# Optimization experiments

Hardware: AMD Instinct MI355X
Metric: run time of the kernel (lower is better)

## Reference

```python
import jax, jax.numpy as jnp
import numpy as np

RATIO = 0.2
OLD_CL = 11

def setup_inputs() -> dict:
    key = jax.random.key(0)
    inputs = jax.random.normal(key, (8, 19, 512, 1024), dtype=jnp.float32)
    return {"inputs": inputs}

def reference(inputs):
    N, C, H, W = inputs.shape
    probs = jax.nn.softmax(inputs, axis=1)              # (N,C,H,W)
    argpred = jnp.argmax(probs, axis=1)                 # (N,H,W) int
    # Per-image class histogram via one segment_sum: segment id = n*C + class
    flat = argpred.reshape(N, H * W)
    ids = (flat + (jnp.arange(N, dtype=flat.dtype)[:, None] * C)).reshape(-1)
    hist = jax.ops.segment_sum(jnp.ones((N * H * W,), jnp.float32), ids,
                               num_segments=N * C).reshape(N, C)
    hist = jnp.where(hist == 0, 1.0, hist)              # hist[hist==0]=1
    weight = jnp.power(hist.sum(axis=1, keepdims=True) / hist, RATIO)  # (N,C)
    if OLD_CL > 0:
        weight = weight.at[:, :OLD_CL].set(1.0)
    weight = jax.lax.stop_gradient(weight)[:, :, None, None]  # (N,C,1,1), detached
    loss = -(probs * probs) * weight
    return loss.mean()
```

## Files before the change

kernel.cpp:

```cpp
#include <hip/hip_runtime.h>

#define NIMG 8
#define NC 19
#define HW (512*1024)
#define BPI 128
#define TPB 256
#define ITERS 8
#define CPB (ITERS*TPB)
#define OLD_CL 11
#define NWAVE (TPB/64)

typedef float    f32x2 __attribute__((ext_vector_type(2)));
typedef unsigned u32x2 __attribute__((ext_vector_type(2)));

__global__ __launch_bounds__(TPB, 4) void iw_main(const float* __restrict__ in,
                                                  float* __restrict__ sPart,
                                                  unsigned* __restrict__ hPart) {
    const int b   = blockIdx.x;
    const int n   = b >> 7;
    const int bl  = b & (BPI - 1);
    const int tid = threadIdx.x;
    const float* img = in + (size_t)n * NC * HW;

    float    acc[NC];
    unsigned hc[5];
#pragma unroll
    for (int c = 0; c < NC; ++c) acc[c] = 0.f;
#pragma unroll
    for (int r = 0; r < 5; ++r) hc[r] = 0u;

    const float L2E = 1.4426950408889634f;

    for (int it = 0; it < ITERS; ++it) {
        const int    chunk = bl * CPB + it * TPB + tid;
        const size_t p     = (size_t)chunk * 2;

        float x0[NC], x1[NC];
#pragma unroll
        for (int c = 0; c < NC; ++c) {
            const f32x2 t = *reinterpret_cast<const f32x2*>(img + (size_t)c * HW + p);
            x0[c] = t[0]; x1[c] = t[1];
        }

#define PIXEL(X)                                                              \
        {                                                                     \
            float m = X[0];                                                   \
            _Pragma("unroll")                                                 \
            for (int c = 1; c < NC; ++c) m = fmaxf(m, X[c]);                  \
            int mi = NC - 1;                                                  \
            _Pragma("unroll")                                                 \
            for (int c = NC - 2; c >= 0; --c) mi = (X[c] == m) ? c : mi;      \
            {                                                                 \
                const unsigned inc = 1u << ((mi & 3) * 8);                    \
                const int r = mi >> 2;                                        \
                hc[0] += (r == 0) ? inc : 0u;                                 \
                hc[1] += (r == 1) ? inc : 0u;                                 \
                hc[2] += (r == 2) ? inc : 0u;                                 \
                hc[3] += (r == 3) ? inc : 0u;                                 \
                hc[4] += (r == 4) ? inc : 0u;                                 \
            }                                                                 \
            const float ml = m * L2E;                                         \
            float e[NC]; float d = 0.f;                                       \
            _Pragma("unroll")                                                 \
            for (int c = 0; c < NC; ++c) {                                    \
                e[c] = exp2f(fmaf(X[c], L2E, -ml));                           \
                d += e[c];                                                    \
            }                                                                 \
            const float inv  = __builtin_amdgcn_rcpf(d);                      \
            const float inv2 = inv * inv;                                     \
            _Pragma("unroll")                                                 \
            for (int c = 0; c < NC; ++c)                                      \
                acc[c] = fmaf(e[c] * e[c], inv2, acc[c]);                     \
        }

        PIXEL(x0); PIXEL(x1);
#undef PIXEL
    }

    unsigned hu[NC];
#pragma unroll
    for (int c = 0; c < NC; ++c) hu[c] = (hc[c >> 2] >> ((c & 3) * 8)) & 0xFFu;

#pragma unroll
    for (int c = 0; c < NC; ++c) {
#pragma unroll
        for (int off = 32; off >= 1; off >>= 1) {
            acc[c] += __shfl_xor(acc[c], off, 64);
            hu[c]  += (unsigned)__shfl_xor((int)hu[c], off, 64);
        }
    }

    __shared__ float    ls[NWAVE][NC];
    __shared__ unsigned lh[NWAVE][NC];
    const int wave = tid >> 6;
    const int lane = tid & 63;
    if (lane == 0) {
#pragma unroll
        for (int c = 0; c < NC; ++c) { ls[wave][c] = acc[c]; lh[wave][c] = hu[c]; }
    }
    __syncthreads();
    if (tid < NC) {
        float s = 0.f; unsigned h = 0u;
#pragma unroll
        for (int w = 0; w < NWAVE; ++w) { s += ls[w][tid]; h += lh[w][tid]; }
        sPart[(size_t)tid * (NIMG * BPI) + n * BPI + bl] = s;
        hPart[(size_t)tid * (NIMG * BPI) + n * BPI + bl] = h;
    }
}

__global__ __launch_bounds__(1024) void iw_final(const float* __restrict__ sPart,
                                                 const unsigned* __restrict__ hPart,
                                                 float* __restrict__ out) {
    __shared__ float    sRed[NIMG * NC];
    __shared__ unsigned hRed[NIMG * NC];
    __shared__ double contrib[NIMG * NC];
    __shared__ double histL[NIMG * NC];
    __shared__ double hsum[NIMG];

    const int t    = threadIdx.x;
    const int wv   = t >> 6;
    const int lane = t & 63;

#pragma unroll
    for (int i = 0; i < 10; ++i) {
        const int pair = wv + 16 * i;
        if (pair < NIMG * NC) {
            const size_t base = (size_t)pair * BPI + lane * 2;
            const f32x2 sv = *reinterpret_cast<const f32x2*>(sPart + base);
            const u32x2 hv = *reinterpret_cast<const u32x2*>(hPart + base);
            float    s = sv[0] + sv[1];
            unsigned h = hv[0] + hv[1];
#pragma unroll
            for (int off = 32; off >= 1; off >>= 1) {
                s += __shfl_xor(s, off, 64);
                h += (unsigned)__shfl_xor((int)h, off, 64);
            }
            if (lane == 0) { sRed[pair] = s; hRed[pair] = h; }
        }
    }
    __syncthreads();

    if (t < NIMG * NC) {
        const int c = t / NIMG, n = t % NIMG;
        const int idx = n * NC + c;
        const unsigned h = hRed[t];
        histL[idx]   = (h == 0u) ? 1.0 : (double)h;
        contrib[idx] = (double)sRed[t];
    }
    __syncthreads();
    if (t < NIMG) {
        double hs = 0.0;
        for (int c = 0; c < NC; ++c) hs += histL[t * NC + c];
        hsum[t] = hs;
    }
    __syncthreads();
    if (t < NIMG * NC) {
        const int n = t / NC, c = t % NC;
        const double w = (c < OLD_CL) ? 1.0 : pow(hsum[n] / histL[t], 0.2);
        contrib[t] = w * contrib[t];
    }
    __syncthreads();
    if (t == 0) {
        double tot = 0.0;
        for (int i = 0; i < NIMG * NC; ++i) tot += contrib[i];
        out[0] = (float)(-tot / (double)((size_t)NIMG * NC * HW));
    }
}

extern "C" void kernel_launch(void* const* d_in, const int* in_sizes, int n_in,
                              void* d_out, int out_size, void* d_ws, size_t ws_size,
                              hipStream_t stream) {
    const float* in = (const float*)d_in[0];
    float* out = (float*)d_out;

    float*    sPart = (float*)d_ws;
    unsigned* hPart = (unsigned*)((char*)d_ws + (size_t)NC * NIMG * BPI * sizeof(float));

    iw_main<<<dim3(NIMG * BPI), TPB, 0, stream>>>(in, sPart, hPart);
    iw_final<<<1, 1024, 0, stream>>>(sPart, hPart, out);
}
```

Measured before the change: 69.82 us.

## Stage channel tiles through LDS with direct global-to-LDS 16-byte loads

```diff
diff --git a/kernel.cpp b/kernel.cpp
--- a/kernel.cpp
+++ b/kernel.cpp
@@ -1,26 +1,35 @@
 #include <hip/hip_runtime.h>
+#include <stdint.h>
 
 #define NIMG 8
 #define NC 19
 #define HW (512*1024)
 #define BPI 128
 #define TPB 256
-#define ITERS 8
-#define CPB (ITERS*TPB)
+#define TILE 512
+#define NTILE 8
 #define OLD_CL 11
 #define NWAVE (TPB/64)
 
 typedef float    f32x2 __attribute__((ext_vector_type(2)));
 typedef unsigned u32x2 __attribute__((ext_vector_type(2)));
+
+typedef const __attribute__((address_space(1))) uint32_t glb_u32;
+typedef __attribute__((address_space(3))) uint32_t       lds_u32;
 
 __global__ __launch_bounds__(TPB, 4) void iw_main(const float* __restrict__ in,
                                                   float* __restrict__ sPart,
                                                   unsigned* __restrict__ hPart) {
-    const int b   = blockIdx.x;
-    const int n   = b >> 7;
-    const int bl  = b & (BPI - 1);
-    const int tid = threadIdx.x;
-    const float* img = in + (size_t)n * NC * HW;
+    __shared__ float tile[NC * TILE];
+
+    const int b    = blockIdx.x;
+    const int n    = b >> 7;
+    const int bl   = b & (BPI - 1);
+    const int tid  = threadIdx.x;
+    const int wave = tid >> 6;
+    const int lane = tid & 63;
+
+    const float* img = in + (size_t)n * NC * HW + (size_t)bl * (NTILE * TILE);
 
     float    acc[NC];
     unsigned hc[5];
@@ -31,15 +40,24 @@
 
     const float L2E = 1.4426950408889634f;
 
-    for (int it = 0; it < ITERS; ++it) {
-        const int    chunk = bl * CPB + it * TPB + tid;
-        const size_t p     = (size_t)chunk * 2;
+    const int c0 = wave * 5;
+    const int cn = (wave == 3) ? 4 : 5;
+
+    for (int t = 0; t < NTILE; ++t) {
+        for (int ci = 0; ci < cn; ++ci) {
+            const int c = c0 + ci;
+            const float* gp = img + (size_t)c * HW + t * TILE + lane * 4;
+            float*       lp = &tile[c * TILE];
+            __builtin_amdgcn_global_load_lds((glb_u32*)gp,         (lds_u32*)lp,         16, 0, 0);
+            __builtin_amdgcn_global_load_lds((glb_u32*)(gp + 256), (lds_u32*)(lp + 256), 16, 0, 0);
+        }
+        __syncthreads();
 
         float x0[NC], x1[NC];
 #pragma unroll
         for (int c = 0; c < NC; ++c) {
-            const f32x2 t = *reinterpret_cast<const f32x2*>(img + (size_t)c * HW + p);
-            x0[c] = t[0]; x1[c] = t[1];
+            const f32x2 v = *reinterpret_cast<const f32x2*>(&tile[c * TILE + 2 * tid]);
+            x0[c] = v[0]; x1[c] = v[1];
         }
 
 #define PIXEL(X)                                                              \
@@ -75,6 +93,8 @@
 
         PIXEL(x0); PIXEL(x1);
 #undef PIXEL
+
+        __syncthreads();
     }
 
     unsigned hu[NC];
@@ -90,19 +110,18 @@
         }
     }
 
-    __shared__ float    ls[NWAVE][NC];
-    __shared__ unsigned lh[NWAVE][NC];
-    const int wave = tid >> 6;
-    const int lane = tid & 63;
+    __syncthreads();
+    float*    ls = tile;
+    unsigned* lh = (unsigned*)(tile + NWAVE * NC);
     if (lane == 0) {
 #pragma unroll
-        for (int c = 0; c < NC; ++c) { ls[wave][c] = acc[c]; lh[wave][c] = hu[c]; }
+        for (int c = 0; c < NC; ++c) { ls[wave * NC + c] = acc[c]; lh[wave * NC + c] = hu[c]; }
     }
     __syncthreads();
     if (tid < NC) {
         float s = 0.f; unsigned h = 0u;
 #pragma unroll
-        for (int w = 0; w < NWAVE; ++w) { s += ls[w][tid]; h += lh[w][tid]; }
+        for (int w = 0; w < NWAVE; ++w) { s += ls[w * NC + tid]; h += lh[w * NC + tid]; }
         sPart[(size_t)tid * (NIMG * BPI) + n * BPI + bl] = s;
         hPart[(size_t)tid * (NIMG * BPI) + n * BPI + bl] = h;
     }
```

Result: slower. 73.80 us (+5.7%).

## Fuse final reduction into main kernel via last-block atomic counter

Applied to the files above, without the earlier changes.

```diff
diff --git a/kernel.cpp b/kernel.cpp
--- a/kernel.cpp
+++ b/kernel.cpp
@@ -1,4 +1,5 @@
 #include <hip/hip_runtime.h>
+#include <stdint.h>
 
 #define NIMG 8
 #define NC 19
@@ -9,17 +10,24 @@
 #define CPB (ITERS*TPB)
 #define OLD_CL 11
 #define NWAVE (TPB/64)
+#define PAIRS (NC*NIMG)
+#define NBLK  (NIMG*BPI)
 
 typedef float    f32x2 __attribute__((ext_vector_type(2)));
-typedef unsigned u32x2 __attribute__((ext_vector_type(2)));
+typedef float    f32x4 __attribute__((ext_vector_type(4)));
+typedef unsigned u32x4 __attribute__((ext_vector_type(4)));
 
-__global__ __launch_bounds__(TPB, 4) void iw_main(const float* __restrict__ in,
-                                                  float* __restrict__ sPart,
-                                                  unsigned* __restrict__ hPart) {
-    const int b   = blockIdx.x;
-    const int n   = b >> 7;
-    const int bl  = b & (BPI - 1);
-    const int tid = threadIdx.x;
+__global__ __launch_bounds__(TPB, 4) void iw_fused(const float* __restrict__ in,
+                                                   float* __restrict__ sPart,
+                                                   unsigned* __restrict__ hPart,
+                                                   unsigned* __restrict__ counter,
+                                                   float* __restrict__ out) {
+    const int b    = blockIdx.x;
+    const int n    = b >> 7;
+    const int bl   = b & (BPI - 1);
+    const int tid  = threadIdx.x;
+    const int wave = tid >> 6;
+    const int lane = tid & 63;
     const float* img = in + (size_t)n * NC * HW;
 
     float    acc[NC];
@@ -80,7 +88,6 @@
     unsigned hu[NC];
 #pragma unroll
     for (int c = 0; c < NC; ++c) hu[c] = (hc[c >> 2] >> ((c & 3) * 8)) & 0xFFu;
-
 #pragma unroll
     for (int c = 0; c < NC; ++c) {
 #pragma unroll
@@ -92,8 +99,6 @@
 
     __shared__ float    ls[NWAVE][NC];
     __shared__ unsigned lh[NWAVE][NC];
-    const int wave = tid >> 6;
-    const int lane = tid & 63;
     if (lane == 0) {
 #pragma unroll
         for (int c = 0; c < NC; ++c) { ls[wave][c] = acc[c]; lh[wave][c] = hu[c]; }
@@ -103,66 +108,60 @@
         float s = 0.f; unsigned h = 0u;
 #pragma unroll
         for (int w = 0; w < NWAVE; ++w) { s += ls[w][tid]; h += lh[w][tid]; }
-        sPart[(size_t)tid * (NIMG * BPI) + n * BPI + bl] = s;
-        hPart[(size_t)tid * (NIMG * BPI) + n * BPI + bl] = h;
-    }
-}
-
-__global__ __launch_bounds__(1024) void iw_final(const float* __restrict__ sPart,
-                                                 const unsigned* __restrict__ hPart,
-                                                 float* __restrict__ out) {
-    __shared__ float    sRed[NIMG * NC];
-    __shared__ unsigned hRed[NIMG * NC];
-    __shared__ double contrib[NIMG * NC];
-    __shared__ double histL[NIMG * NC];
-    __shared__ double hsum[NIMG];
-
-    const int t    = threadIdx.x;
-    const int wv   = t >> 6;
-    const int lane = t & 63;
-
-#pragma unroll
-    for (int i = 0; i < 10; ++i) {
-        const int pair = wv + 16 * i;
-        if (pair < NIMG * NC) {
-            const size_t base = (size_t)pair * BPI + lane * 2;
-            const f32x2 sv = *reinterpret_cast<const f32x2*>(sPart + base);
-            const u32x2 hv = *reinterpret_cast<const u32x2*>(hPart + base);
-            float    s = sv[0] + sv[1];
-            unsigned h = hv[0] + hv[1];
-#pragma unroll
-            for (int off = 32; off >= 1; off >>= 1) {
-                s += __shfl_xor(s, off, 64);
-                h += (unsigned)__shfl_xor((int)h, off, 64);
-            }
-            if (lane == 0) { sRed[pair] = s; hRed[pair] = h; }
-        }
+        __hip_atomic_store(&sPart[(size_t)tid * (NIMG * BPI) + n * BPI + bl], s,
+                           __ATOMIC_RELAXED, __HIP_MEMORY_SCOPE_AGENT);
+        __hip_atomic_store(&hPart[(size_t)tid * (NIMG * BPI) + n * BPI + bl], h,
+                           __ATOMIC_RELAXED, __HIP_MEMORY_SCOPE_AGENT);
     }
     __syncthreads();
 
-    if (t < NIMG * NC) {
-        const int c = t / NIMG, n = t % NIMG;
-        const int idx = n * NC + c;
-        const unsigned h = hRed[t];
-        histL[idx]   = (h == 0u) ? 1.0 : (double)h;
-        contrib[idx] = (double)sRed[t];
+    __shared__ unsigned isLast;
+    if (tid == 0) {
+        __threadfence();
+        const unsigned t = __hip_atomic_fetch_add(counter, 1u,
+                              __ATOMIC_ACQ_REL, __HIP_MEMORY_SCOPE_AGENT);
+        isLast = (t == NBLK - 1) ? 1u : 0u;
     }
     __syncthreads();
-    if (t < NIMG) {
-        double hs = 0.0;
-        for (int c = 0; c < NC; ++c) hs += histL[t * NC + c];
-        hsum[t] = hs;
+    if (!isLast) return;
+    __threadfence();
+
+    __shared__ double histL[PAIRS];
+    __shared__ double contrib[PAIRS];
+    __shared__ double hsum[NIMG];
+
+    double S = 0.0; unsigned Hc = 0u;
+    if (tid < PAIRS) {
+        const float*    sp = sPart + (size_t)tid * BPI;
+        const unsigned* hp = hPart + (size_t)tid * BPI;
+#pragma unroll 8
+        for (int j = 0; j < BPI; j += 4) {
+            const f32x4 sv = *reinterpret_cast<const f32x4*>(sp + j);
+            const u32x4 hv = *reinterpret_cast<const u32x4*>(hp + j);
+            S  += (double)sv[0] + (double)sv[1] + (double)sv[2] + (double)sv[3];
+            Hc += hv[0] + hv[1] + hv[2] + hv[3];
+        }
+        const int c  = tid / NIMG, n2 = tid % NIMG;
+        const int idx = n2 * NC + c;
+        histL[idx]   = (Hc == 0u) ? 1.0 : (double)Hc;
+        contrib[idx] = S;
     }
     __syncthreads();
-    if (t < NIMG * NC) {
-        const int n = t / NC, c = t % NC;
-        const double w = (c < OLD_CL) ? 1.0 : pow(hsum[n] / histL[t], 0.2);
-        contrib[t] = w * contrib[t];
+    if (tid < NIMG) {
+        double hs = 0.0;
+        for (int c = 0; c < NC; ++c) hs += histL[tid * NC + c];
+        hsum[tid] = hs;
     }
     __syncthreads();
-    if (t == 0) {
+    if (tid < PAIRS) {
+        const int n2 = tid / NC, c = tid % NC;
+        const double w = (c < OLD_CL) ? 1.0 : pow(hsum[n2] / histL[tid], 0.2);
+        contrib[tid] = w * contrib[tid];
+    }
+    __syncthreads();
+    if (tid == 0) {
         double tot = 0.0;
-        for (int i = 0; i < NIMG * NC; ++i) tot += contrib[i];
+        for (int i = 0; i < PAIRS; ++i) tot += contrib[i];
         out[0] = (float)(-tot / (double)((size_t)NIMG * NC * HW));
     }
 }
@@ -170,12 +169,13 @@
 extern "C" void kernel_launch(void* const* d_in, const int* in_sizes, int n_in,
                               void* d_out, int out_size, void* d_ws, size_t ws_size,
                               hipStream_t stream) {
-    const float* in = (const float*)d_in[0];
-    float* out = (float*)d_out;
+    const float* in  = (const float*)d_in[0];
+    float*       out = (float*)d_out;
 
-    float*    sPart = (float*)d_ws;
-    unsigned* hPart = (unsigned*)((char*)d_ws + (size_t)NC * NIMG * BPI * sizeof(float));
+    float*    sPart   = (float*)d_ws;
+    unsigned* hPart   = (unsigned*)((char*)d_ws + (size_t)PAIRS * BPI * sizeof(float));
+    unsigned* counter = (unsigned*)((char*)d_ws + (size_t)PAIRS * BPI * sizeof(float) * 2);
 
-    iw_main<<<dim3(NIMG * BPI), TPB, 0, stream>>>(in, sPart, hPart);
-    iw_final<<<1, 1024, 0, stream>>>(sPart, hPart, out);
+    hipMemsetAsync(counter, 0, sizeof(unsigned), stream);
+    iw_fused<<<dim3(NBLK), TPB, 0, stream>>>(in, sPart, hPart, counter, out);
 }
```

Result: slower. 148.9 us (+113.3%).
